# Kernel optimization log

Hardware: AMD Instinct MI355X
Metric: run time of the kernel (lower is better)

## Reference

```python
import jax, jax.numpy as jnp
import numpy as np

BS, NUM_PATCH, N_VARS, PATCH_LEN, D_MODEL = 32, 64, 321, 12, 128
TIME_RATIO, FREQ_RATIO = 0.5, 0.4


def setup_inputs() -> dict:
    key = jax.random.key(0)
    ks = jax.random.split(key, 7)
    x = jax.random.normal(ks[0], (BS, NUM_PATCH, N_VARS, PATCH_LEN), jnp.float32)
    W_in = jax.random.normal(ks[1], (PATCH_LEN, D_MODEL), jnp.float32) / np.sqrt(PATCH_LEN)
    b_in = jnp.zeros((D_MODEL,), jnp.float32)
    W_out = jax.random.normal(ks[2], (D_MODEL, PATCH_LEN), jnp.float32) / np.sqrt(D_MODEL)
    b_out = jnp.zeros((PATCH_LEN,), jnp.float32)
    # nn.Parameter(torch.zeros(1,1,1)) in the original; use small random scalars so grads are non-trivial
    time_mask_token = jax.random.normal(ks[3], (), jnp.float32) * 0.02
    freq_mask_token = jax.random.normal(ks[4], (), jnp.float32) * 0.02
    return {"x": x, "W_in": W_in, "b_in": b_in, "W_out": W_out, "b_out": b_out,
            "time_mask_token": time_mask_token, "freq_mask_token": freq_mask_token}


def _scatter_mask(idx, num_patch):
    # idx: [bs, n_vars, k] patch indices to mask (set False). Returns bool [bs, num_patch, n_vars].
    bs, nv, k = idx.shape
    m = jnp.ones((bs, num_patch, nv), dtype=bool)
    b = jnp.arange(bs)[:, None, None]
    v = jnp.arange(nv)[None, :, None]
    return m.at[b, idx, v].set(False)


def reference(x, W_in, b_in, W_out, b_out, time_mask_token, freq_mask_token):
    bs, num_patch, n_vars, patch_len = x.shape

    # patch2emb applied per token (equivalent to the gather-encode path since the
    # projection is pointwise per patch): [bs, np, nv, d_model]
    emb = jnp.einsum('bpvl,ld->bpvd', x, W_in) + b_in

    # ---- time masking: mask patches with highest coefficient of variation ----
    cv = jnp.std(x, axis=-1, ddof=1) / (jnp.mean(x, axis=-1) + 1e-6)  # [bs, np, nv]
    k_t = int(num_patch * TIME_RATIO)
    _, idx_t = jax.lax.top_k(jnp.transpose(cv, (0, 2, 1)), k_t)       # [bs, nv, k_t]
    mask_t = _scatter_mask(idx_t, num_patch)                           # True = keep
    tokens_t = jnp.where(mask_t[..., None], emb, time_mask_token)
    out_t = jnp.einsum('bpvd,dl->bpvl', tokens_t, W_out) + b_out

    # ---- freq masking: mask patches with lowest mean FFT magnitude ----
    mag = jnp.abs(jnp.fft.rfft(x, axis=-1))                            # [bs, np, nv, pl//2+1]
    score = mag.mean(axis=-1)                                          # [bs, np, nv]
    k_f = int(num_patch * FREQ_RATIO)
    _, idx_f = jax.lax.top_k(-jnp.transpose(score, (0, 2, 1)), k_f)    # smallest scores
    mask_f = _scatter_mask(idx_f, num_patch)
    tokens_f = jnp.where(mask_f[..., None], emb, freq_mask_token)
    out_f = jnp.einsum('bpvd,dl->bpvl', tokens_f, W_out) + b_out

    return out_t * 0.5 + out_f * 0.5
```

## Files before the change

### kernel.cpp

```cpp
#include <hip/hip_runtime.h>
#include <math.h>

constexpr int BS = 32, NP = 64, NV = 321, PL = 12, DM = 128;
constexpr int KT = 32;
constexpr int KF = 25;
constexpr int VB = 8;
constexpr int NCHUNK = 41;
constexpr int RSTRIDE = 64 * 13 + 4;

__device__ __forceinline__ unsigned ord(float f) {
  unsigned u = __float_as_uint(f);
  return ((int)u < 0) ? ~u : (u | 0x80000000u);
}

__global__ void prep_kernel(const float* __restrict__ W_in,
                            const float* __restrict__ b_in,
                            const float* __restrict__ W_out,
                            const float* __restrict__ tt,
                            const float* __restrict__ ft,
                            float* __restrict__ prep) {
  int t = threadIdx.x;
  if (t < 144) {
    int i = t / 12, l = t % 12;
    const float4* Wi = (const float4*)(W_in + i * DM);
    float s = 0.f;
#pragma unroll 8
    for (int d4 = 0; d4 < 32; ++d4) {
      float4 a = Wi[d4];
      const float* wo = W_out + d4 * 48 + l;
      s += a.x * wo[0] + a.y * wo[12] + a.z * wo[24] + a.w * wo[36];
    }
    prep[t] = s;
  } else if (t < 168) {
    int l = (t - 144) % 12;
    float cs = 0.f, cb = 0.f;
#pragma unroll 8
    for (int d = 0; d < DM; ++d) {
      float w = W_out[d * 12 + l];
      cs += w;
      cb += b_in[d] * w;
    }
    if (t < 156) {
      prep[144 + l] = cb;
      prep[156 + l] = tt[0] * cs;
    } else {
      prep[168 + l] = ft[0] * cs;
    }
  }
}

__global__ __launch_bounds__(256) void fused_kernel(
    const float* __restrict__ x, const float* __restrict__ b_out,
    const float* __restrict__ prep, float* __restrict__ out) {
  __shared__ float xs[VB * RSTRIDE];
  __shared__ __align__(16) float spp[192];
  __shared__ unsigned long long smT[VB], smF[VB];

  const int t = threadIdx.x;
  const int chunk = blockIdx.x;
  const int b = blockIdx.y;
  const int v0 = chunk * VB;
  const bool full = (chunk < 40);
  const int nv = full ? VB : 1;

  const float* xb = x + ((size_t)(b * 64) * NV + v0) * PL;

  float4 r0[2], r1[2], r2[2];
  int ofs[2] = {0, 0};
  if (full) {
#pragma unroll
    for (int h = 0; h < 2; ++h) {
      const int j = t + h * 256;
      const int p = j >> 3, vv = j & 7;
      const float4* src = (const float4*)(xb + ((size_t)p * NV + vv) * PL);
      r0[h] = src[0];
      r1[h] = src[1];
      r2[h] = src[2];
      ofs[h] = vv * RSTRIDE + p * 13;
    }
  } else if (t < 64) {
    const float4* src = (const float4*)(xb + (size_t)t * NV * PL);
    r0[0] = src[0];
    r1[0] = src[1];
    r2[0] = src[2];
    ofs[0] = t * 13;
  }

  if (t < 180) spp[t] = prep[t];
  else if (t < 192) spp[t] = b_out[t - 180];

  if (full) {
#pragma unroll
    for (int h = 0; h < 2; ++h) {
      float* d = xs + ofs[h];
      d[0] = r0[h].x; d[1] = r0[h].y; d[2] = r0[h].z; d[3] = r0[h].w;
      d[4] = r1[h].x; d[5] = r1[h].y; d[6] = r1[h].z; d[7] = r1[h].w;
      d[8] = r2[h].x; d[9] = r2[h].y; d[10] = r2[h].z; d[11] = r2[h].w;
    }
  } else if (t < 64) {
    float* d = xs + ofs[0];
    d[0] = r0[0].x; d[1] = r0[0].y; d[2] = r0[0].z; d[3] = r0[0].w;
    d[4] = r1[0].x; d[5] = r1[0].y; d[6] = r1[0].z; d[7] = r1[0].w;
    d[8] = r2[0].x; d[9] = r2[0].y; d[10] = r2[0].z; d[11] = r2[0].w;
  }
  __syncthreads();

  const int wv = t >> 6, lane = t & 63;
  const float H = 0.86602540378443864676f;
#pragma unroll
  for (int k = 0; k < 2; ++k) {
    const int vv = wv * 2 + k;
    if (vv < nv) {
      const float* xp = xs + vv * RSTRIDE + lane * 13;
      float xv[12];
#pragma unroll
      for (int i = 0; i < 12; ++i) xv[i] = xp[i];

      float s = 0.f;
#pragma unroll
      for (int i = 0; i < 12; ++i) s += xv[i];
      const float m = s * (1.0f / 12.0f);
      float ss = 0.f;
#pragma unroll
      for (int i = 0; i < 12; ++i) {
        float d = xv[i] - m;
        ss += d * d;
      }
      const float cv = sqrtf(ss * (1.0f / 11.0f)) / (m + 1e-6f);

      const float e1 = xv[1] + xv[11], e2 = xv[2] + xv[10], e3 = xv[3] + xv[9],
                  e4 = xv[4] + xv[8], e5 = xv[5] + xv[7];
      const float o1 = xv[1] - xv[11], o2 = xv[2] - xv[10], o3 = xv[3] - xv[9],
                  o4 = xv[4] - xv[8], o5 = xv[5] - xv[7];
      float mag = fabsf(xv[0] + xv[6] + e1 + e2 + e3 + e4 + e5);
      float re = xv[0] - xv[6] + H * (e1 - e5) + 0.5f * (e2 - e4);
      float im = 0.5f * (o1 + o5) + H * (o2 + o4) + o3;
      mag += sqrtf(re * re + im * im);
      re = xv[0] + xv[6] + 0.5f * (e1 + e5) - 0.5f * (e2 + e4) - e3;
      im = H * (o1 + o2 - o4 - o5);
      mag += sqrtf(re * re + im * im);
      re = xv[0] - xv[6] - e2 + e4;
      im = o1 - o3 + o5;
      mag += sqrtf(re * re + im * im);
      re = xv[0] + xv[6] - 0.5f * (e1 + e2 + e4 + e5) + e3;
      im = H * (o1 - o2 + o4 - o5);
      mag += sqrtf(re * re + im * im);
      re = xv[0] - xv[6] + H * (e5 - e1) + 0.5f * (e2 - e4);
      im = 0.5f * (o1 + o5) - H * (o2 + o4) + o3;
      mag += sqrtf(re * re + im * im);
      re = xv[0] + xv[6] - e1 + e2 - e3 + e4 - e5;
      mag += fabsf(re);
      const float fs = mag * (1.0f / 7.0f);

      const unsigned ut = ord(cv);
      const unsigned uf = ~ord(fs);
      unsigned tht = 0, thf = 0;
#pragma unroll
      for (int bit = 31; bit >= 0; --bit) {
        const unsigned ct = tht | (1u << bit);
        const unsigned cf = thf | (1u << bit);
        const unsigned long long bt = __ballot(ut >= ct);
        const unsigned long long bf = __ballot(uf >= cf);
        if (__popcll(bt) >= KT) tht = ct;
        if (__popcll(bf) >= KF) thf = cf;
      }
      const unsigned long long pre = (1ull << lane) - 1ull;
      const int gt_t = __popcll(__ballot(ut > tht));
      const int rt = __popcll(__ballot(ut == tht) & pre);
      const bool masked_t = (ut > tht) || ((ut == tht) && (rt < KT - gt_t));
      const int gt_f = __popcll(__ballot(uf > thf));
      const int rf = __popcll(__ballot(uf == thf) & pre);
      const bool masked_f = (uf > thf) || ((uf == thf) && (rf < KF - gt_f));
      const unsigned long long bkt = __ballot(!masked_t);
      const unsigned long long bkf = __ballot(!masked_f);
      if (lane == 0) {
        smT[vv] = bkt;
        smF[vv] = bkf;
      }
    }
  }
  __syncthreads();

  const float* sM = spp;
  const float* sc = spp + 144;
  const float* sSt = spp + 156;
  const float* sSf = spp + 168;
  const float* sb = spp + 180;
  const int p2 = t >> 2;
  const int vv0 = (t & 3) * 2;
  const bool val0 = vv0 < nv, val1 = (vv0 + 1) < nv;
  float xv2[2][12], E[2][12];
#pragma unroll
  for (int j = 0; j < 2; ++j) {
    const float* xp = xs + (vv0 + j) * RSTRIDE + p2 * 13;
#pragma unroll
    for (int i = 0; i < 12; ++i) xv2[j][i] = xp[i];
  }
#pragma unroll
  for (int l = 0; l < 12; ++l) {
    E[0][l] = sc[l];
    E[1][l] = sc[l];
  }
  const float4* M4 = (const float4*)sM;
#pragma unroll
  for (int i = 0; i < 12; ++i) {
    float4 m0 = M4[i * 3], m1 = M4[i * 3 + 1], m2 = M4[i * 3 + 2];
    float a0 = xv2[0][i], a1 = xv2[1][i];
    E[0][0] += a0 * m0.x;  E[0][1] += a0 * m0.y;
    E[0][2] += a0 * m0.z;  E[0][3] += a0 * m0.w;
    E[0][4] += a0 * m1.x;  E[0][5] += a0 * m1.y;
    E[0][6] += a0 * m1.z;  E[0][7] += a0 * m1.w;
    E[0][8] += a0 * m2.x;  E[0][9] += a0 * m2.y;
    E[0][10] += a0 * m2.z; E[0][11] += a0 * m2.w;
    E[1][0] += a1 * m0.x;  E[1][1] += a1 * m0.y;
    E[1][2] += a1 * m0.z;  E[1][3] += a1 * m0.w;
    E[1][4] += a1 * m1.x;  E[1][5] += a1 * m1.y;
    E[1][6] += a1 * m1.z;  E[1][7] += a1 * m1.w;
    E[1][8] += a1 * m2.x;  E[1][9] += a1 * m2.y;
    E[1][10] += a1 * m2.z; E[1][11] += a1 * m2.w;
  }
#pragma unroll
  for (int j = 0; j < 2; ++j) {
    if (j == 0 ? val0 : val1) {
      const int vv = vv0 + j;
      const bool kt = (smT[vv] >> p2) & 1ull;
      const bool kf = (smF[vv] >> p2) & 1ull;
      float o[12];
#pragma unroll
      for (int l = 0; l < 12; ++l) {
        float e = E[j][l];
        float at = kt ? e : sSt[l];
        float af = kf ? e : sSf[l];
        o[l] = 0.5f * (at + af) + sb[l];
      }
      float* op = out + ((size_t)(b * 64 + p2) * NV + v0 + vv) * PL;
      ((float4*)op)[0] = make_float4(o[0], o[1], o[2], o[3]);
      ((float4*)op)[1] = make_float4(o[4], o[5], o[6], o[7]);
      ((float4*)op)[2] = make_float4(o[8], o[9], o[10], o[11]);
    }
  }
}

extern "C" void kernel_launch(void* const* d_in, const int* in_sizes, int n_in,
                              void* d_out, int out_size, void* d_ws,
                              size_t ws_size, hipStream_t stream) {
  const float* x = (const float*)d_in[0];
  const float* W_in = (const float*)d_in[1];
  const float* b_in = (const float*)d_in[2];
  const float* W_out = (const float*)d_in[3];
  const float* b_out = (const float*)d_in[4];
  const float* tt = (const float*)d_in[5];
  const float* ft = (const float*)d_in[6];
  float* out = (float*)d_out;
  float* prep = (float*)d_ws;

  hipLaunchKernelGGL(prep_kernel, dim3(1), dim3(192), 0, stream, W_in, b_in,
                     W_out, tt, ft, prep);
  hipLaunchKernelGGL(fused_kernel, dim3(NCHUNK, BS), dim3(256), 0, stream, x,
                     b_out, prep, out);
}
```

Baseline: 120.0 us.

## Keep x patches in registers and stage only per-patch scores in LDS

Each thread now keeps its loaded x patches in registers and uses them for the score computation and the projection. Before, the whole 8-variable tile was staged in shared memory and read back twice. Only the CV and FFT scores go to shared memory, so the wave-per-variable top-k selection still works, and the output is written by the thread that loaded the input. This cuts LDS traffic and footprint, which may raise occupancy, at the cost of more live registers per thread. b_out is also folded into the prep buffer so it arrives with a single load.

```diff
diff --git a/kernel.cpp b/kernel.cpp
--- a/kernel.cpp
+++ b/kernel.cpp
@@ -1,12 +1,12 @@
 #include <hip/hip_runtime.h>
 #include <math.h>
 
-constexpr int BS = 32, NP = 64, NV = 321, PL = 12, DM = 128;
+constexpr int BS = 32, NV = 321, PL = 12, DM = 128;
 constexpr int KT = 32;
 constexpr int KF = 25;
 constexpr int VB = 8;
 constexpr int NCHUNK = 41;
-constexpr int RSTRIDE = 64 * 13 + 4;
+constexpr int SST = 72;
 
 __device__ __forceinline__ unsigned ord(float f) {
   unsigned u = __float_as_uint(f);
@@ -16,6 +16,7 @@
 __global__ void prep_kernel(const float* __restrict__ W_in,
                             const float* __restrict__ b_in,
                             const float* __restrict__ W_out,
+                            const float* __restrict__ b_out,
                             const float* __restrict__ tt,
                             const float* __restrict__ ft,
                             float* __restrict__ prep) {
@@ -46,13 +47,16 @@
     } else {
       prep[168 + l] = ft[0] * cs;
     }
+  } else if (t < 180) {
+    prep[180 + (t - 168)] = b_out[t - 168];
   }
 }
 
 __global__ __launch_bounds__(256) void fused_kernel(
-    const float* __restrict__ x, const float* __restrict__ b_out,
-    const float* __restrict__ prep, float* __restrict__ out) {
-  __shared__ float xs[VB * RSTRIDE];
+    const float* __restrict__ x, const float* __restrict__ prep,
+    float* __restrict__ out) {
+  __shared__ float scv[VB * SST];
+  __shared__ float sfs[VB * SST];
   __shared__ __align__(16) float spp[192];
   __shared__ unsigned long long smT[VB], smF[VB];
 
@@ -65,57 +69,43 @@
 
   const float* xb = x + ((size_t)(b * 64) * NV + v0) * PL;
 
-  float4 r0[2], r1[2], r2[2];
-  int ofs[2] = {0, 0};
+  float xr[2][12];
+  int pp[2], vvv[2];
   if (full) {
 #pragma unroll
     for (int h = 0; h < 2; ++h) {
-      const int j = t + h * 256;
+      const int j = t + 256 * h;
       const int p = j >> 3, vv = j & 7;
+      pp[h] = p;
+      vvv[h] = vv;
       const float4* src = (const float4*)(xb + ((size_t)p * NV + vv) * PL);
-      r0[h] = src[0];
-      r1[h] = src[1];
-      r2[h] = src[2];
-      ofs[h] = vv * RSTRIDE + p * 13;
-    }
-  } else if (t < 64) {
-    const float4* src = (const float4*)(xb + (size_t)t * NV * PL);
-    r0[0] = src[0];
-    r1[0] = src[1];
-    r2[0] = src[2];
-    ofs[0] = t * 13;
-  }
-
-  if (t < 180) spp[t] = prep[t];
-  else if (t < 192) spp[t] = b_out[t - 180];
-
-  if (full) {
-#pragma unroll
-    for (int h = 0; h < 2; ++h) {
-      float* d = xs + ofs[h];
-      d[0] = r0[h].x; d[1] = r0[h].y; d[2] = r0[h].z; d[3] = r0[h].w;
-      d[4] = r1[h].x; d[5] = r1[h].y; d[6] = r1[h].z; d[7] = r1[h].w;
-      d[8] = r2[h].x; d[9] = r2[h].y; d[10] = r2[h].z; d[11] = r2[h].w;
-    }
-  } else if (t < 64) {
-    float* d = xs + ofs[0];
-    d[0] = r0[0].x; d[1] = r0[0].y; d[2] = r0[0].z; d[3] = r0[0].w;
-    d[4] = r1[0].x; d[5] = r1[0].y; d[6] = r1[0].z; d[7] = r1[0].w;
-    d[8] = r2[0].x; d[9] = r2[0].y; d[10] = r2[0].z; d[11] = r2[0].w;
-  }
-  __syncthreads();
-
-  const int wv = t >> 6, lane = t & 63;
+      float4 a = src[0], bb = src[1], c = src[2];
+      xr[h][0] = a.x;  xr[h][1] = a.y;  xr[h][2] = a.z;  xr[h][3] = a.w;
+      xr[h][4] = bb.x; xr[h][5] = bb.y; xr[h][6] = bb.z; xr[h][7] = bb.w;
+      xr[h][8] = c.x;  xr[h][9] = c.y;  xr[h][10] = c.z; xr[h][11] = c.w;
+    }
+  } else {
+    pp[0] = t & 63;
+    vvv[0] = 0;
+    pp[1] = 0;
+    vvv[1] = 0;
+    if (t < 64) {
+      const float4* src = (const float4*)(xb + (size_t)t * NV * PL);
+      float4 a = src[0], bb = src[1], c = src[2];
+      xr[0][0] = a.x;  xr[0][1] = a.y;  xr[0][2] = a.z;  xr[0][3] = a.w;
+      xr[0][4] = bb.x; xr[0][5] = bb.y; xr[0][6] = bb.z; xr[0][7] = bb.w;
+      xr[0][8] = c.x;  xr[0][9] = c.y;  xr[0][10] = c.z; xr[0][11] = c.w;
+    }
+  }
+
+  if (t < 192) spp[t] = prep[t];
+
   const float H = 0.86602540378443864676f;
 #pragma unroll
-  for (int k = 0; k < 2; ++k) {
-    const int vv = wv * 2 + k;
-    if (vv < nv) {
-      const float* xp = xs + vv * RSTRIDE + lane * 13;
-      float xv[12];
-#pragma unroll
-      for (int i = 0; i < 12; ++i) xv[i] = xp[i];
-
+  for (int h = 0; h < 2; ++h) {
+    const bool valid = full || (h == 0 && t < 64);
+    if (valid) {
+      const float* xv = xr[h];
       float s = 0.f;
 #pragma unroll
       for (int i = 0; i < 12; ++i) s += xv[i];
@@ -152,8 +142,19 @@
       mag += fabsf(re);
       const float fs = mag * (1.0f / 7.0f);
 
-      const unsigned ut = ord(cv);
-      const unsigned uf = ~ord(fs);
+      scv[vvv[h] * SST + pp[h]] = cv;
+      sfs[vvv[h] * SST + pp[h]] = fs;
+    }
+  }
+  __syncthreads();
+
+  const int wv = t >> 6, lane = t & 63;
+#pragma unroll
+  for (int k = 0; k < 2; ++k) {
+    const int vv = wv * 2 + k;
+    if (vv < nv) {
+      const unsigned ut = ord(scv[vv * SST + lane]);
+      const unsigned uf = ~ord(sfs[vv * SST + lane]);
       unsigned tht = 0, thf = 0;
 #pragma unroll
       for (int bit = 31; bit >= 0; --bit) {
@@ -181,59 +182,47 @@
   }
   __syncthreads();
 
-  const float* sM = spp;
-  const float* sc = spp + 144;
-  const float* sSt = spp + 156;
-  const float* sSf = spp + 168;
-  const float* sb = spp + 180;
-  const int p2 = t >> 2;
-  const int vv0 = (t & 3) * 2;
-  const bool val0 = vv0 < nv, val1 = (vv0 + 1) < nv;
-  float xv2[2][12], E[2][12];
-#pragma unroll
-  for (int j = 0; j < 2; ++j) {
-    const float* xp = xs + (vv0 + j) * RSTRIDE + p2 * 13;
-#pragma unroll
-    for (int i = 0; i < 12; ++i) xv2[j][i] = xp[i];
-  }
+  float E0[12], E1[12];
 #pragma unroll
   for (int l = 0; l < 12; ++l) {
-    E[0][l] = sc[l];
-    E[1][l] = sc[l];
-  }
-  const float4* M4 = (const float4*)sM;
+    E0[l] = spp[144 + l];
+    E1[l] = spp[144 + l];
+  }
+  const float4* M4 = (const float4*)spp;
 #pragma unroll
   for (int i = 0; i < 12; ++i) {
     float4 m0 = M4[i * 3], m1 = M4[i * 3 + 1], m2 = M4[i * 3 + 2];
-    float a0 = xv2[0][i], a1 = xv2[1][i];
-    E[0][0] += a0 * m0.x;  E[0][1] += a0 * m0.y;
-    E[0][2] += a0 * m0.z;  E[0][3] += a0 * m0.w;
-    E[0][4] += a0 * m1.x;  E[0][5] += a0 * m1.y;
-    E[0][6] += a0 * m1.z;  E[0][7] += a0 * m1.w;
-    E[0][8] += a0 * m2.x;  E[0][9] += a0 * m2.y;
-    E[0][10] += a0 * m2.z; E[0][11] += a0 * m2.w;
-    E[1][0] += a1 * m0.x;  E[1][1] += a1 * m0.y;
-    E[1][2] += a1 * m0.z;  E[1][3] += a1 * m0.w;
-    E[1][4] += a1 * m1.x;  E[1][5] += a1 * m1.y;
-    E[1][6] += a1 * m1.z;  E[1][7] += a1 * m1.w;
-    E[1][8] += a1 * m2.x;  E[1][9] += a1 * m2.y;
-    E[1][10] += a1 * m2.z; E[1][11] += a1 * m2.w;
-  }
-#pragma unroll
-  for (int j = 0; j < 2; ++j) {
-    if (j == 0 ? val0 : val1) {
-      const int vv = vv0 + j;
-      const bool kt = (smT[vv] >> p2) & 1ull;
-      const bool kf = (smF[vv] >> p2) & 1ull;
+    float a0 = xr[0][i], a1 = xr[1][i];
+    E0[0] += a0 * m0.x;  E0[1] += a0 * m0.y;
+    E0[2] += a0 * m0.z;  E0[3] += a0 * m0.w;
+    E0[4] += a0 * m1.x;  E0[5] += a0 * m1.y;
+    E0[6] += a0 * m1.z;  E0[7] += a0 * m1.w;
+    E0[8] += a0 * m2.x;  E0[9] += a0 * m2.y;
+    E0[10] += a0 * m2.z; E0[11] += a0 * m2.w;
+    E1[0] += a1 * m0.x;  E1[1] += a1 * m0.y;
+    E1[2] += a1 * m0.z;  E1[3] += a1 * m0.w;
+    E1[4] += a1 * m1.x;  E1[5] += a1 * m1.y;
+    E1[6] += a1 * m1.z;  E1[7] += a1 * m1.w;
+    E1[8] += a1 * m2.x;  E1[9] += a1 * m2.y;
+    E1[10] += a1 * m2.z; E1[11] += a1 * m2.w;
+  }
+#pragma unroll
+  for (int h = 0; h < 2; ++h) {
+    const bool valid = full || (h == 0 && t < 64);
+    if (valid) {
+      const int p = pp[h], vv = vvv[h];
+      const bool kt = (smT[vv] >> p) & 1ull;
+      const bool kf = (smF[vv] >> p) & 1ull;
+      const float* E = (h == 0) ? E0 : E1;
       float o[12];
 #pragma unroll
       for (int l = 0; l < 12; ++l) {
-        float e = E[j][l];
-        float at = kt ? e : sSt[l];
-        float af = kf ? e : sSf[l];
-        o[l] = 0.5f * (at + af) + sb[l];
-      }
-      float* op = out + ((size_t)(b * 64 + p2) * NV + v0 + vv) * PL;
+        float e = E[l];
+        float at = kt ? e : spp[156 + l];
+        float af = kf ? e : spp[168 + l];
+        o[l] = 0.5f * (at + af) + spp[180 + l];
+      }
+      float* op = out + ((size_t)(b * 64 + p) * NV + v0 + vv) * PL;
       ((float4*)op)[0] = make_float4(o[0], o[1], o[2], o[3]);
       ((float4*)op)[1] = make_float4(o[4], o[5], o[6], o[7]);
       ((float4*)op)[2] = make_float4(o[8], o[9], o[10], o[11]);
@@ -255,7 +244,7 @@
   float* prep = (float*)d_ws;
 
   hipLaunchKernelGGL(prep_kernel, dim3(1), dim3(192), 0, stream, W_in, b_in,
-                     W_out, tt, ft, prep);
+                     W_out, b_out, tt, ft, prep);
   hipLaunchKernelGGL(fused_kernel, dim3(NCHUNK, BS), dim3(256), 0, stream, x,
-                     b_out, prep, out);
-}
+                     prep, out);
+}
```

Result: faster. 117.2 us (-2.3%).
